# Kernel optimization log

Hardware: AMD Instinct MI355X
Metric: run time of the kernel (lower is better)

Reference implementation:

```python
import jax, jax.numpy as jnp
import numpy as np

N = 32768        # out_features
K = 8192         # in_features
GROUP_SIZE = 128
G = K // GROUP_SIZE   # groups per row = 64
KP = K // 8           # packed bytes per row = 1024


def setup_inputs() -> dict:
    key = jax.random.key(0)
    k1, k2, k3 = jax.random.split(key, 3)
    x = jax.random.normal(k1, (1, K), dtype=jnp.float32).astype(jnp.float16)
    # packed sign bits: one uint8 holds 8 signs (bit i -> column k*8+i)
    packed_signs = jax.random.randint(k2, (N, KP), 0, 256, dtype=jnp.int32).astype(jnp.uint8)
    # per-(row, group) scales = mean |w| over each group of 128 weights (positive fp16)
    scales = (jax.random.uniform(k3, (N, G), dtype=jnp.float32) * 0.05 + 0.005).astype(jnp.float16)
    return {"x": x, "packed_signs": packed_signs, "scales": scales}


def _unpack_signs(packed_signs):
    # [N, KP] uint8 -> [N, K] float32 in {-1, +1}; bit i is weight column kb*8+i
    bits = (packed_signs[:, :, None] >> jnp.arange(8, dtype=jnp.uint8)[None, None, :]) & jnp.uint8(1)
    n, kp, _ = bits.shape
    return bits.reshape(n, kp * 8).astype(jnp.float32) * 2.0 - 1.0


def reference(x, packed_signs, scales):
    # out[b, n] = sum_k sign[n, k] * scale[n, k // group_size] * x[b, k]
    n, kp = packed_signs.shape
    k = kp * 8
    g = scales.shape[1]
    gs = k // g
    signs = _unpack_signs(packed_signs)                     # [N, K]
    xg = x.reshape(-1, g, gs).astype(jnp.float32)           # [B, G, gs]
    # per-group sign dot-products, then weight by the group scale
    partial = jnp.einsum('ngj,bgj->bng', signs.reshape(n, g, gs), xg)  # [B, N, G]
    out = jnp.einsum('bng,ng->bn', partial, scales.astype(jnp.float32))
    return out.astype(jnp.float16)                          # [1, N], fp16 like the kernel
```

## Files before the change

kernel.cpp:

```cpp
#include <hip/hip_runtime.h>
#include <hip/hip_bf16.h>
#include <hip/hip_fp16.h>

#define NROWS   32768
#define KTOT    8192
#define KP      1024
#define GROUPS  64

#define SLICE_W 256
#define SLICE_B 32
#define NSLICES (KTOT / SLICE_W)
#define BLK     512
#define ROWS_PER_BLK 512
#define CHUNKS  (NROWS / ROWS_PER_BLK)

__global__ __launch_bounds__(BLK, 8)
void bitlin_partials(const float* __restrict__ x,
                     const int* __restrict__ packed,
                     __half2* __restrict__ pTh)
{
    __shared__ float lut[SLICE_B][256];

    const int s     = blockIdx.x & (NSLICES - 1);
    const int chunk = blockIdx.x >> 5;
    const int tid   = threadIdx.x;

    {
        const int pos = tid >> 4;
        const int b0  = (tid & 15) << 4;
        float xs[8];
#pragma unroll
        for (int i = 0; i < 8; ++i)
            xs[i] = x[s * SLICE_W + pos * 8 + i];
#pragma unroll
        for (int b = 0; b < 16; ++b) {
            const int byte = b0 + b;
            float v = 0.f;
#pragma unroll
            for (int i = 0; i < 8; ++i)
                v += ((byte >> i) & 1) ? xs[i] : -xs[i];
            lut[pos][byte] = v;
        }
    }
    __syncthreads();

    const int lane = tid & 63;
    const int wave = tid >> 6;
    const int sub  = lane & 7;
    const int rsub = lane >> 3;
    const int rowBase = chunk * ROWS_PER_BLK + wave * 64;

    const int4* __restrict__ p4 = (const int4*)packed;

#pragma unroll
    for (int t = 0; t < 8; ++t) {
        const int r = rowBase + t * 8 + rsub;
        const int4 v = p4[r * (KP / 4) + s * (SLICE_B / 4) + sub];
        const int pos0 = sub * 4;
        float acc = lut[pos0 + 0][v.x & 255]
                  + lut[pos0 + 1][v.y & 255]
                  + lut[pos0 + 2][v.z & 255]
                  + lut[pos0 + 3][v.w & 255];
        acc += __shfl_xor(acc, 1);
        acc += __shfl_xor(acc, 2);
        const float accOdd = __shfl_xor(acc, 4);
        if (sub == 0)
            pTh[(size_t)s * NROWS + r] = __floats2half2_rn(acc, accOdd);
    }
}

__global__ __launch_bounds__(512)
void bitlin_scale(const __half2* __restrict__ pTh,
                  const float* __restrict__ scales,
                  float* __restrict__ out)
{
    __shared__ float s_s[64][65];
    __shared__ float s_part[64][9];

    const int tid     = threadIdx.x;
    const int lane    = tid & 63;
    const int wave    = tid >> 6;
    const int rowBase = blockIdx.x * 64;

    const float4* s4 = (const float4*)(scales + (size_t)rowBase * GROUPS);
#pragma unroll
    for (int i = 0; i < 2; ++i) {
        const int idx = i * 512 + tid;
        const float4 v = s4[idx];
        const int r = idx >> 4;
        const int c = (idx & 15) * 4;
        s_s[r][c + 0] = v.x;
        s_s[r][c + 1] = v.y;
        s_s[r][c + 2] = v.z;
        s_s[r][c + 3] = v.w;
    }
    __syncthreads();

    const int r = rowBase + lane;
    float acc = 0.f;
#pragma unroll
    for (int i = 0; i < 4; ++i) {
        const int s = wave * 4 + i;
        const float2 f = __half22float2(pTh[(size_t)s * NROWS + r]);
        acc += f.x * s_s[lane][s * 2] + f.y * s_s[lane][s * 2 + 1];
    }
    s_part[lane][wave] = acc;
    __syncthreads();

    if (wave == 0) {
        float a = 0.f;
#pragma unroll
        for (int w = 0; w < 8; ++w) a += s_part[lane][w];
        out[r] = a;
    }
}

__global__ __launch_bounds__(BLK, 4)
void bitlin_main_atomic(const float* __restrict__ x,
                        const int* __restrict__ packed,
                        const float* __restrict__ scales,
                        float* __restrict__ ws)
{
    __shared__ float lut[SLICE_B][256];
    const int s     = blockIdx.x & (NSLICES - 1);
    const int chunk = blockIdx.x >> 5;
    const int tid   = threadIdx.x;
    {
        const int pos = tid >> 4;
        const int b0  = (tid & 15) << 4;
        float xs[8];
#pragma unroll
        for (int i = 0; i < 8; ++i)
            xs[i] = x[s * SLICE_W + pos * 8 + i];
#pragma unroll
        for (int b = 0; b < 16; ++b) {
            const int byte = b0 + b;
            float v = 0.f;
#pragma unroll
            for (int i = 0; i < 8; ++i)
                v += ((byte >> i) & 1) ? xs[i] : -xs[i];
            lut[pos][byte] = v;
        }
    }
    __syncthreads();

    const int lane = tid & 63;
    const int wave = tid >> 6;
    const int sub  = lane & 7;
    const int rsub = lane >> 3;
    const int rowBase = chunk * ROWS_PER_BLK + wave * 64;
    const int4* __restrict__ p4 = (const int4*)packed;

#pragma unroll
    for (int t = 0; t < 8; ++t) {
        const int r = rowBase + t * 8 + rsub;
        const int4 v = p4[r * (KP / 4) + s * (SLICE_B / 4) + sub];
        const float sc = scales[r * GROUPS + s * 2 + (sub >> 2)];
        const int pos0 = sub * 4;
        float acc = lut[pos0 + 0][v.x & 255]
                  + lut[pos0 + 1][v.y & 255]
                  + lut[pos0 + 2][v.z & 255]
                  + lut[pos0 + 3][v.w & 255];
        acc *= sc;
        acc += __shfl_xor(acc, 1);
        acc += __shfl_xor(acc, 2);
        acc += __shfl_xor(acc, 4);
        if (sub == 0) atomicAdd(&ws[r], acc);
    }
}

__global__ __launch_bounds__(512)
void bitlin_fin(const float* __restrict__ ws, float* __restrict__ out)
{
    const int i = blockIdx.x * blockDim.x + threadIdx.x;
    out[i] = ws[i];
}

extern "C" void kernel_launch(void* const* d_in, const int* in_sizes, int n_in,
                              void* d_out, int out_size, void* d_ws, size_t ws_size,
                              hipStream_t stream)
{
    const float* x      = (const float*)d_in[0];
    const int*   packed = (const int*)d_in[1];
    const float* scales = (const float*)d_in[2];

    const size_t pTh_bytes = (size_t)NSLICES * NROWS * sizeof(__half2);

    if (ws_size >= pTh_bytes) {
        __half2* pTh = (__half2*)d_ws;
        bitlin_partials<<<dim3(NSLICES * CHUNKS), dim3(BLK), 0, stream>>>(x, packed, pTh);
        bitlin_scale<<<dim3(NROWS / 64), dim3(512), 0, stream>>>(pTh, scales, (float*)d_out);
    } else {
        float* ws = (float*)d_ws;
        hipMemsetAsync(ws, 0, NROWS * sizeof(float), stream);
        bitlin_main_atomic<<<dim3(NSLICES * CHUNKS), dim3(BLK), 0, stream>>>(x, packed, scales, ws);
        bitlin_fin<<<dim3(NROWS / 512), dim3(512), 0, stream>>>(ws, (float*)d_out);
    }
}
```

Before: 31.18 us.

## Build LUT by Gray-code walk, double rows per block, store per-group half partials

The LUT build now walks a Gray-code sequence, so each thread does incremental adds in place of 16 full 8-term sums, and the LUT rows are padded to 264 to reduce bank conflicts. Each block now covers 1024 rows, so the LUT build cost is spread over twice the work, with a partially unrolled 16-iteration loop. Partials are written as one half per group (two shuffles in place of three, two lanes storing), and the scale kernel reads eight group halves per wave. Each block now takes longer and there are half as many, which lowers parallelism, and the partial stores become narrower and more scattered.

```diff
diff --git a/kernel.cpp b/kernel.cpp
--- a/kernel.cpp
+++ b/kernel.cpp
@@ -1,5 +1,4 @@
 #include <hip/hip_runtime.h>
-#include <hip/hip_bf16.h>
 #include <hip/hip_fp16.h>
 
 #define NROWS   32768
@@ -11,15 +10,16 @@
 #define SLICE_B 32
 #define NSLICES (KTOT / SLICE_W)
 #define BLK     512
-#define ROWS_PER_BLK 512
-#define CHUNKS  (NROWS / ROWS_PER_BLK)
+#define ROWS_PER_BLK 1024
+#define RCHUNKS (NROWS / ROWS_PER_BLK)
+#define LUTPAD  264
 
 __global__ __launch_bounds__(BLK, 8)
 void bitlin_partials(const float* __restrict__ x,
                      const int* __restrict__ packed,
-                     __half2* __restrict__ pTh)
-{
-    __shared__ float lut[SLICE_B][256];
+                     __half* __restrict__ pTh)
+{
+    __shared__ float lut[SLICE_B][LUTPAD];
 
     const int s     = blockIdx.x & (NSLICES - 1);
     const int chunk = blockIdx.x >> 5;
@@ -27,20 +27,34 @@
 
     {
         const int pos = tid >> 4;
-        const int b0  = (tid & 15) << 4;
+        const int L   = tid & 15;
         float xs[8];
 #pragma unroll
-        for (int i = 0; i < 8; ++i)
-            xs[i] = x[s * SLICE_W + pos * 8 + i];
-#pragma unroll
-        for (int b = 0; b < 16; ++b) {
-            const int byte = b0 + b;
-            float v = 0.f;
-#pragma unroll
-            for (int i = 0; i < 8; ++i)
-                v += ((byte >> i) & 1) ? xs[i] : -xs[i];
-            lut[pos][byte] = v;
-        }
+        for (int i = 0; i < 8; ++i) xs[i] = x[s * SLICE_W + pos * 8 + i];
+        float e = ((L & 1) ? xs[0] : -xs[0])
+                + ((L & 2) ? xs[1] : -xs[1])
+                + ((L & 4) ? xs[2] : -xs[2])
+                + ((L & 8) ? xs[3] : -xs[3])
+                - xs[4] - xs[5] - xs[6] - xs[7];
+        const float t0 = 2.f * xs[4], t1 = 2.f * xs[5],
+                    t2 = 2.f * xs[6], t3 = 2.f * xs[7];
+        float* row = &lut[pos][L];
+        row[ 0*16] = e;
+        e += t0; row[ 1*16] = e;
+        e += t1; row[ 3*16] = e;
+        e -= t0; row[ 2*16] = e;
+        e += t2; row[ 6*16] = e;
+        e += t0; row[ 7*16] = e;
+        e -= t1; row[ 5*16] = e;
+        e -= t0; row[ 4*16] = e;
+        e += t3; row[12*16] = e;
+        e += t0; row[13*16] = e;
+        e += t1; row[15*16] = e;
+        e -= t0; row[14*16] = e;
+        e -= t2; row[10*16] = e;
+        e += t0; row[11*16] = e;
+        e -= t1; row[ 9*16] = e;
+        e -= t0; row[ 8*16] = e;
     }
     __syncthreads();
 
@@ -48,12 +62,12 @@
     const int wave = tid >> 6;
     const int sub  = lane & 7;
     const int rsub = lane >> 3;
-    const int rowBase = chunk * ROWS_PER_BLK + wave * 64;
+    const int rowBase = chunk * ROWS_PER_BLK + wave * (ROWS_PER_BLK / 8);
 
     const int4* __restrict__ p4 = (const int4*)packed;
 
-#pragma unroll
-    for (int t = 0; t < 8; ++t) {
+#pragma unroll 4
+    for (int t = 0; t < 16; ++t) {
         const int r = rowBase + t * 8 + rsub;
         const int4 v = p4[r * (KP / 4) + s * (SLICE_B / 4) + sub];
         const int pos0 = sub * 4;
@@ -63,14 +77,13 @@
                   + lut[pos0 + 3][v.w & 255];
         acc += __shfl_xor(acc, 1);
         acc += __shfl_xor(acc, 2);
-        const float accOdd = __shfl_xor(acc, 4);
-        if (sub == 0)
-            pTh[(size_t)s * NROWS + r] = __floats2half2_rn(acc, accOdd);
+        if ((sub & 3) == 0)
+            pTh[(s * 2 + (sub >> 2)) * NROWS + r] = __float2half_rn(acc);
     }
 }
 
 __global__ __launch_bounds__(512)
-void bitlin_scale(const __half2* __restrict__ pTh,
+void bitlin_scale(const __half* __restrict__ pTh,
                   const float* __restrict__ scales,
                   float* __restrict__ out)
 {
@@ -99,10 +112,9 @@
     const int r = rowBase + lane;
     float acc = 0.f;
 #pragma unroll
-    for (int i = 0; i < 4; ++i) {
-        const int s = wave * 4 + i;
-        const float2 f = __half22float2(pTh[(size_t)s * NROWS + r]);
-        acc += f.x * s_s[lane][s * 2] + f.y * s_s[lane][s * 2 + 1];
+    for (int i = 0; i < 8; ++i) {
+        const int g = wave * 8 + i;
+        acc += __half2float(pTh[(size_t)g * NROWS + r]) * s_s[lane][g];
     }
     s_part[lane][wave] = acc;
     __syncthreads();
@@ -130,8 +142,7 @@
         const int b0  = (tid & 15) << 4;
         float xs[8];
 #pragma unroll
-        for (int i = 0; i < 8; ++i)
-            xs[i] = x[s * SLICE_W + pos * 8 + i];
+        for (int i = 0; i < 8; ++i) xs[i] = x[s * SLICE_W + pos * 8 + i];
 #pragma unroll
         for (int b = 0; b < 16; ++b) {
             const int byte = b0 + b;
@@ -148,7 +159,7 @@
     const int wave = tid >> 6;
     const int sub  = lane & 7;
     const int rsub = lane >> 3;
-    const int rowBase = chunk * ROWS_PER_BLK + wave * 64;
+    const int rowBase = chunk * 512 + wave * 64;
     const int4* __restrict__ p4 = (const int4*)packed;
 
 #pragma unroll
@@ -184,16 +195,16 @@
     const int*   packed = (const int*)d_in[1];
     const float* scales = (const float*)d_in[2];
 
-    const size_t pTh_bytes = (size_t)NSLICES * NROWS * sizeof(__half2);
+    const size_t pTh_bytes = (size_t)GROUPS * NROWS * sizeof(__half);
 
     if (ws_size >= pTh_bytes) {
-        __half2* pTh = (__half2*)d_ws;
-        bitlin_partials<<<dim3(NSLICES * CHUNKS), dim3(BLK), 0, stream>>>(x, packed, pTh);
+        __half* pTh = (__half*)d_ws;
+        bitlin_partials<<<dim3(NSLICES * RCHUNKS), dim3(BLK), 0, stream>>>(x, packed, pTh);
         bitlin_scale<<<dim3(NROWS / 64), dim3(512), 0, stream>>>(pTh, scales, (float*)d_out);
     } else {
         float* ws = (float*)d_ws;
         hipMemsetAsync(ws, 0, NROWS * sizeof(float), stream);
-        bitlin_main_atomic<<<dim3(NSLICES * CHUNKS), dim3(BLK), 0, stream>>>(x, packed, scales, ws);
+        bitlin_main_atomic<<<dim3(NSLICES * (NROWS / 512)), dim3(BLK), 0, stream>>>(x, packed, scales, ws);
         bitlin_fin<<<dim3(NROWS / 512), dim3(512), 0, stream>>>(ws, (float*)d_out);
     }
 }
```

Measured after the change: 31.84 us. 2.1% more time.
